# Performance work log

Measured on AMD Instinct MI355X. Metric: run time of the kernel, lower is better.

The kernel has to match this reference:

```python
import jax, jax.numpy as jnp
import numpy as np

B, N, DIM, HEADS, DH, EDGE, DEPTH, K = 4, 128, 256, 8, 64, 64, 2, 512
INNER = HEADS * DH
SCALE = DH ** -0.5


def _ln(x, g, b, eps=1e-5):
    m = x.mean(-1, keepdims=True)
    v = ((x - m) ** 2).mean(-1, keepdims=True)
    return (x - m) / jnp.sqrt(v + eps) * g + b


def _rotate_half(x):
    # interleaved pairs: (d r) with r=2 -> (-x2, x1)
    xp = x.reshape(x.shape[:-1] + (-1, 2))
    x1, x2 = xp[..., 0], xp[..., 1]
    return jnp.stack((-x2, x1), axis=-1).reshape(x.shape)


def _gated_res(x, res, gw):
    gate = jax.nn.sigmoid(jnp.concatenate((x, res, x - res), axis=-1) @ gw)
    return x * gate + res * (1 - gate)


def forward(nodes, edges, edge_ln_g, edge_ln_b, ln1_g, ln1_b, w_exp, b_exp,
            w_q, b_q, w_kv, b_kv, w_ekv, b_ekv, w_out, b_out, gate1_w,
            ln2_g, ln2_b, w_ff1, b_ff1, w_ff2, b_ff2, gate2_w, codebook):
    b, n = nodes.shape[:2]
    # LayerNorm edges over channel dim: (B,C,N,N) -> (B,N,N,C)
    e = _ln(jnp.transpose(edges, (0, 2, 3, 1)), edge_ln_g, edge_ln_b)
    # rotary frequencies over positions, repeated pairwise -> (1, N, DH)
    inv = 1.0 / (10000.0 ** (jnp.arange(0, DH, 2, dtype=jnp.float32) / DH))
    fr = jnp.repeat(jnp.arange(n, dtype=jnp.float32)[:, None] * inv[None, :], 2, axis=-1)
    cos, sin = jnp.cos(fr)[None], jnp.sin(fr)[None]

    def heads3(t):  # (B,N,H*D) -> (B*H,N,D)
        return t.reshape(b, n, HEADS, DH).transpose(0, 2, 1, 3).reshape(b * HEADS, n, DH)

    for i in range(DEPTH):
        # PreNorm + edge-conditioned attention
        x = _ln(nodes, ln1_g[i], ln1_b[i])
        x = x @ w_exp[i] + b_exp[i]
        q = x @ w_q[i] + b_q[i]
        k, v = jnp.split(x @ w_kv[i] + b_kv[i], 2, axis=-1)
        ekv = e @ w_ekv[i] + b_ekv[i]  # (B,N,N,INNER)
        q, k, v = heads3(q), heads3(k), heads3(v)
        ekv = ekv.reshape(b, n, n, HEADS, DH).transpose(0, 3, 1, 2, 4).reshape(b * HEADS, n, n, DH)
        q = q * cos + _rotate_half(q) * sin
        k = k * cos + _rotate_half(k) * sin
        kk = k[:, None, :, :] + ekv  # (BH, i, j, d)
        vv = v[:, None, :, :] + ekv
        sim = jnp.einsum('bid,bijd->bij', q, kk) * SCALE
        att = jax.nn.softmax(sim, axis=-1)
        out = jnp.einsum('bij,bijd->bid', att, vv)
        out = out.reshape(b, HEADS, n, DH).transpose(0, 2, 1, 3).reshape(b, n, INNER)
        out = out @ w_out[i] + b_out[i]
        nodes = _gated_res(out, nodes, gate1_w[i])
        # PreNorm + FeedForward
        h = _ln(nodes, ln2_g[i], ln2_b[i])
        h = jax.nn.gelu(h @ w_ff1[i] + b_ff1[i], approximate=False) @ w_ff2[i] + b_ff2[i]
        nodes = _gated_res(h, nodes, gate2_w[i])

    # VQ codebook nearest-neighbor lookup with straight-through estimator
    z = nodes.reshape(-1, DIM)
    d = (z * z).sum(-1, keepdims=True) - 2.0 * z @ codebook.T + (codebook * codebook).sum(-1)[None, :]
    idx = jnp.argmin(d, axis=-1)
    zq = codebook[idx].reshape(b, n, DIM)
    return nodes + jax.lax.stop_gradient(zq - nodes)


def setup_inputs() -> dict:
    key = jax.random.key(0)
    ks = jax.random.split(key, 16)
    s = 0.02
    inp = {
        'nodes': jax.random.normal(ks[0], (B, N, DIM), jnp.float32),
        'edges': jax.random.normal(ks[1], (B, EDGE, N, N), jnp.float32),
        'edge_ln_g': jnp.ones((EDGE,), jnp.float32),
        'edge_ln_b': jnp.zeros((EDGE,), jnp.float32),
        'ln1_g': jnp.ones((DEPTH, DIM), jnp.float32),
        'ln1_b': jnp.zeros((DEPTH, DIM), jnp.float32),
        'w_exp': s * jax.random.normal(ks[2], (DEPTH, DIM, INNER), jnp.float32),
        'b_exp': jnp.zeros((DEPTH, INNER), jnp.float32),
        'w_q': s * jax.random.normal(ks[3], (DEPTH, INNER, INNER), jnp.float32),
        'b_q': jnp.zeros((DEPTH, INNER), jnp.float32),
        'w_kv': s * jax.random.normal(ks[4], (DEPTH, INNER, 2 * INNER), jnp.float32),
        'b_kv': jnp.zeros((DEPTH, 2 * INNER), jnp.float32),
        'w_ekv': s * jax.random.normal(ks[5], (DEPTH, EDGE, INNER), jnp.float32),
        'b_ekv': jnp.zeros((DEPTH, INNER), jnp.float32),
        'w_out': s * jax.random.normal(ks[6], (DEPTH, INNER, DIM), jnp.float32),
        'b_out': jnp.zeros((DEPTH, DIM), jnp.float32),
        'gate1_w': s * jax.random.normal(ks[7], (DEPTH, 3 * DIM, 1), jnp.float32),
        'ln2_g': jnp.ones((DEPTH, DIM), jnp.float32),
        'ln2_b': jnp.zeros((DEPTH, DIM), jnp.float32),
        'w_ff1': s * jax.random.normal(ks[8], (DEPTH, DIM, 4 * DIM), jnp.float32),
        'b_ff1': jnp.zeros((DEPTH, 4 * DIM), jnp.float32),
        'w_ff2': s * jax.random.normal(ks[9], (DEPTH, 4 * DIM, DIM), jnp.float32),
        'b_ff2': jnp.zeros((DEPTH, DIM), jnp.float32),
        'gate2_w': s * jax.random.normal(ks[10], (DEPTH, 3 * DIM, 1), jnp.float32),
        'codebook': jax.random.uniform(ks[11], (K, DIM), jnp.float32, -1.0 / K, 1.0 / K),
    }
    return inp


def reference(nodes, edges, edge_ln_g, edge_ln_b, ln1_g, ln1_b, w_exp, b_exp,
              w_q, b_q, w_kv, b_kv, w_ekv, b_ekv, w_out, b_out, gate1_w,
              ln2_g, ln2_b, w_ff1, b_ff1, w_ff2, b_ff2, gate2_w, codebook):
    return forward(nodes, edges, edge_ln_g, edge_ln_b, ln1_g, ln1_b, w_exp, b_exp,
                   w_q, b_q, w_kv, b_kv, w_ekv, b_ekv, w_out, b_out, gate1_w,
                   ln2_g, ln2_b, w_ff1, b_ff1, w_ff2, b_ff2, gate2_w, codebook)
```

## Files before the change

kernel.cpp:

```cpp
#include <hip/hip_runtime.h>
#include <math.h>


#define DEV __device__ __forceinline__

constexpr int Bn = 4, Nn = 128, DIMn = 256, HEADSn = 8, DHn = 64, EDGEn = 64,
              DEPTHn = 2, Kn = 512, INNERn = 512;
constexpr int QKVW = 1536;
constexpr int PART = 131072;

DEV float wave_reduce_sum(float v) {
#pragma unroll
  for (int m = 32; m >= 1; m >>= 1) v += __shfl_xor(v, m);
  return v;
}

DEV float block_reduce_sum_256(float v, float* red) {
  v = wave_reduce_sum(v);
  int tid = threadIdx.x;
  if ((tid & 63) == 0) red[tid >> 6] = v;
  __syncthreads();
  v = red[0] + red[1] + red[2] + red[3];
  __syncthreads();
  return v;
}

DEV float gelu_exact(float x) {
  return 0.5f * x * (1.f + erff(x * 0.70710678118654752f));
}

__global__ __launch_bounds__(256) void prep_kernel(
    const float* __restrict__ edges, const float* __restrict__ eg,
    const float* __restrict__ eb, float* __restrict__ e,
    float* __restrict__ eT, float* __restrict__ cost, float* __restrict__ sint,
    const float* __restrict__ nodes_in, const float* __restrict__ ln1_g,
    const float* __restrict__ ln1_b, float* __restrict__ xln,
    float* __restrict__ nodes, const float* __restrict__ wek,
    const float* __restrict__ w_out, const float* __restrict__ bek,
    const float* __restrict__ b_out, float* __restrict__ W2,
    float* __restrict__ b_out2) {
  __shared__ float smem[8512];
  int blk = blockIdx.x;
  int tid = threadIdx.x;

  if (blk < 64) {
    int l = blk >> 5, h = (blk >> 2) & 7, nt = blk & 3;
    float* As = smem;
    float* Bs = smem + 4160;
    const float* wekl = wek + (size_t)l * 64 * 512 + h * 64;
    const float* woutl =
        w_out + (size_t)l * 512 * 256 + (size_t)(h * 64) * 256 + nt * 64;
    for (int f = tid; f < 1024; f += 256) {
      int c = f >> 4, d4 = (f & 15) << 2;
      float4 w4 = *(const float4*)(wekl + (size_t)c * 512 + d4);
      As[c * 65 + d4 + 0] = w4.x;
      As[c * 65 + d4 + 1] = w4.y;
      As[c * 65 + d4 + 2] = w4.z;
      As[c * 65 + d4 + 3] = w4.w;
    }
    for (int f = tid; f < 1024; f += 256) {
      int d = f >> 4, n4 = (f & 15) << 2;
      float4 w4 = *(const float4*)(woutl + (size_t)d * 256 + n4);
      Bs[d * 68 + n4 + 0] = w4.x;
      Bs[d * 68 + n4 + 1] = w4.y;
      Bs[d * 68 + n4 + 2] = w4.z;
      Bs[d * 68 + n4 + 3] = w4.w;
    }
    __syncthreads();
    int tx = tid & 15, ty = tid >> 4;
    float acc[4][4] = {};
    for (int d = 0; d < 64; ++d) {
      float4 bv = *(const float4*)&Bs[d * 68 + tx * 4];
#pragma unroll
      for (int u = 0; u < 4; ++u) {
        float a = As[(ty * 4 + u) * 65 + d];
        acc[u][0] += a * bv.x;
        acc[u][1] += a * bv.y;
        acc[u][2] += a * bv.z;
        acc[u][3] += a * bv.w;
      }
    }
#pragma unroll
    for (int u = 0; u < 4; ++u) {
      float4 o = {acc[u][0], acc[u][1], acc[u][2], acc[u][3]};
      *(float4*)(W2 + (size_t)l * 512 * 256 +
                 (size_t)(h * 64 + ty * 4 + u) * 256 + nt * 64 + tx * 4) = o;
    }
  } else if (blk < 72) {
    int t = blk - 64;
    int l = t >> 2, nt = t & 3;
    float* part = smem;
    int nn = tid & 63, kq = tid >> 6;
    const float* wcol = w_out + (size_t)l * 512 * 256 + nt * 64 + nn;
    float acc = 0.f;
    for (int k = kq * 128; k < kq * 128 + 128; ++k)
      acc += bek[l * 512 + k] * wcol[(size_t)k * 256];
    part[tid] = acc;
    __syncthreads();
    if (tid < 64)
      b_out2[l * 256 + nt * 64 + nn] =
          b_out[l * 256 + nt * 64 + nn] + part[nn] + part[64 + nn] +
          part[128 + nn] + part[192 + nn];
  } else if (blk < 584) {
    float* ets = smem;
    int eidx = blk - 72;
    int i = eidx & 127, b = eidx >> 7;
    int j = tid & 127;
    bool act = tid < 128;
    if (act) {
      const float* src = edges + (size_t)b * EDGEn * Nn * Nn + i * Nn + j;
      float vals[EDGEn];
      float s = 0.f;
#pragma unroll
      for (int c = 0; c < EDGEn; ++c) {
        float x = src[(size_t)c * (Nn * Nn)];
        vals[c] = x;
        s += x;
      }
      float m = s * (1.0f / 64.0f);
      float s2 = 0.f;
#pragma unroll
      for (int c = 0; c < EDGEn; ++c) {
        float d = vals[c] - m;
        s2 += d * d;
      }
      float inv = 1.f / sqrtf(s2 * (1.0f / 64.0f) + 1e-5f);
      float* dst = e + ((size_t)(b * Nn + i) * EDGEn) * Nn + j;
#pragma unroll
      for (int c = 0; c < EDGEn; ++c) {
        float o = (vals[c] - m) * inv * eg[c] + eb[c];
        dst[(size_t)c * Nn] = o;
        ets[j * 65 + c] = o;
      }
    }
    __syncthreads();
    if (act) {
      float* dstT = eT + ((size_t)(b * Nn + i) * Nn) * EDGEn;
#pragma unroll
      for (int it = 0; it < 16; ++it) {
        int f4 = it * 128 + j;
        int jj = f4 >> 4, c4 = (f4 & 15) << 2;
        float4 o4 = {ets[jj * 65 + c4], ets[jj * 65 + c4 + 1],
                     ets[jj * 65 + c4 + 2], ets[jj * 65 + c4 + 3]};
        *(float4*)(dstT + (size_t)jj * EDGEn + c4) = o4;
      }
    }
  } else if (blk < 600) {
    int t = (blk - 584) * 256 + tid;
    if (t < Nn * 32) {
      int n = t >> 5, p = t & 31;
      float inv = powf(10000.f, -(float)(2 * p) / 64.f);
      float fr = (float)n * inv;
      cost[t] = cosf(fr);
      sint[t] = sinf(fr);
    }
  } else {
    float* red = smem;
    int row = blk - 600;
    float v = nodes_in[(size_t)row * DIMn + tid];
    nodes[(size_t)row * DIMn + tid] = v;
    float m = block_reduce_sum_256(v, red) * (1.0f / 256.0f);
    float d = v - m;
    float var = block_reduce_sum_256(d * d, red) * (1.0f / 256.0f);
    float inv = 1.f / sqrtf(var + 1e-5f);
    xln[(size_t)row * DIMn + tid] = d * inv * ln1_g[tid] + ln1_b[tid];
  }
}

__global__ __launch_bounds__(256) void gemm_kernel(
    const float* __restrict__ A, const float* __restrict__ A2, int aact,
    const float* __restrict__ W1, int N1, const float* __restrict__ b1,
    const float* __restrict__ W2n, int N2, const float* __restrict__ b2,
    const float* __restrict__ Wkb, int Ksplit, float* __restrict__ C, int M,
    int Ntot, int K, int kspan, int act, const float* __restrict__ cost,
    const float* __restrict__ sint, float* __restrict__ kT) {
  __shared__ float As[32][34];
  __shared__ __align__(16) float Bs[32][68];
  int tid = threadIdx.x;
  int bx = blockIdx.x, by = blockIdx.y, zid = blockIdx.z;
  int tx = tid & 15, ty = tid >> 4;
  int arow = tid >> 3, acol = (tid & 7) << 2;
  int brow = tid >> 4, bcol = (tid & 15) << 2;
  int col0 = bx * 64;
  const float* W = W1;
  const float* bias = b1;
  int Nw = N1, wcol = col0;
  if (W2n && col0 >= N1) {
    W = W2n;
    bias = b2;
    Nw = N2;
    wcol = col0 - N1;
  }
  int kb = zid * kspan, kend = kb + kspan;
  const float* arp = A + (size_t)(by * 32 + arow) * K;
  const float* arp2 = A2 ? A2 + (size_t)(by * 32 + arow) * K : nullptr;

  auto load_a = [&](int kpos) -> float4 {
    float4 a = *(const float4*)(arp + kpos + acol);
    if (arp2) {
      float4 a2 = *(const float4*)(arp2 + kpos + acol);
      a.x += a2.x;
      a.y += a2.y;
      a.z += a2.z;
      a.w += a2.w;
    }
    if (aact == 1) {
      a.x = gelu_exact(a.x);
      a.y = gelu_exact(a.y);
      a.z = gelu_exact(a.z);
      a.w = gelu_exact(a.w);
    }
    return a;
  };

  float4 a_nxt = load_a(kb);
  const float* w0p;
  const float* w1p;
  {
    int kr0 = kb + brow, kr1 = kb + brow + 16;
    w0p = (Ksplit && kr0 >= Ksplit)
              ? Wkb + (size_t)(kr0 - Ksplit) * Nw + wcol + bcol
              : W + (size_t)kr0 * Nw + wcol + bcol;
    w1p = (Ksplit && kr1 >= Ksplit)
              ? Wkb + (size_t)(kr1 - Ksplit) * Nw + wcol + bcol
              : W + (size_t)kr1 * Nw + wcol + bcol;
  }
  float4 b0_nxt = *(const float4*)w0p;
  float4 b1_nxt = *(const float4*)w1p;

  float acc[2][4] = {};
  for (int k0 = kb; k0 < kend; k0 += 32) {
    As[acol + 0][arow] = a_nxt.x;
    As[acol + 1][arow] = a_nxt.y;
    As[acol + 2][arow] = a_nxt.z;
    As[acol + 3][arow] = a_nxt.w;
    *(float4*)&Bs[brow][bcol] = b0_nxt;
    *(float4*)&Bs[brow + 16][bcol] = b1_nxt;
    __syncthreads();
    int kn = k0 + 32;
    if (kn < kend) {
      a_nxt = load_a(kn);
      int kr0 = kn + brow, kr1 = kn + brow + 16;
      w0p = (Ksplit && kr0 >= Ksplit)
                ? Wkb + (size_t)(kr0 - Ksplit) * Nw + wcol + bcol
                : W + (size_t)kr0 * Nw + wcol + bcol;
      w1p = (Ksplit && kr1 >= Ksplit)
                ? Wkb + (size_t)(kr1 - Ksplit) * Nw + wcol + bcol
                : W + (size_t)kr1 * Nw + wcol + bcol;
      b0_nxt = *(const float4*)w0p;
      b1_nxt = *(const float4*)w1p;
    }
#pragma unroll
    for (int kk = 0; kk < 32; ++kk) {
      float2 av = *(const float2*)&As[kk][ty * 2];
      float4 bv = *(const float4*)&Bs[kk][tx * 4];
      acc[0][0] += av.x * bv.x;
      acc[0][1] += av.x * bv.y;
      acc[0][2] += av.x * bv.z;
      acc[0][3] += av.x * bv.w;
      acc[1][0] += av.y * bv.x;
      acc[1][1] += av.y * bv.y;
      acc[1][2] += av.y * bv.z;
      acc[1][3] += av.y * bv.w;
    }
    __syncthreads();
  }
  int ccol = wcol + tx * 4;
  bool ksec = (act == 4) && (col0 >= 512) && (col0 < 1024);
  float* trans = (float*)Bs;
  float* Cz = C + (size_t)zid * M * Ntot;
#pragma unroll
  for (int u = 0; u < 2; ++u) {
    int r = by * 32 + ty * 2 + u;
    float o[4];
#pragma unroll
    for (int w = 0; w < 4; ++w)
      o[w] = acc[u][w] + (zid == 0 ? bias[ccol + w] : 0.f);
    if (act == 1) {
#pragma unroll
      for (int w = 0; w < 4; ++w) o[w] = gelu_exact(o[w]);
    } else if (act == 4 && col0 < 1024) {
      int n = r & 127;
      int p0 = (ccol & 63) >> 1;
      float c0 = cost[n * 32 + p0], s0 = sint[n * 32 + p0];
      float c1 = cost[n * 32 + p0 + 1], s1 = sint[n * 32 + p0 + 1];
      float x0 = o[0], x1 = o[1], x2 = o[2], x3 = o[3];
      o[0] = x0 * c0 - x1 * s0;
      o[1] = x1 * c0 + x0 * s0;
      o[2] = x2 * c1 - x3 * s1;
      o[3] = x3 * c1 + x2 * s1;
    }
    if (ksec) {
      int jl = ty * 2 + u;
#pragma unroll
      for (int w = 0; w < 4; ++w) trans[(tx * 4 + w) * 33 + jl] = o[w];
    } else {
      float4 o4 = {o[0], o[1], o[2], o[3]};
      *(float4*)(Cz + (size_t)r * Ntot + col0 + tx * 4) = o4;
    }
  }
  if (ksec) {
    __syncthreads();
    int h = (col0 - 512) >> 6;
    int bb = (by * 32) >> 7;
#pragma unroll
    for (int q = 0; q < 2; ++q) {
      int f4 = tid * 2 + q;
      int dl = f4 >> 3, j4 = (f4 & 7) << 2;
      int jj = (by * 32 + j4) & 127;
      float4 o4 = {trans[dl * 33 + j4], trans[dl * 33 + j4 + 1],
                   trans[dl * 33 + j4 + 2], trans[dl * 33 + j4 + 3]};
      *(float4*)(kT + ((size_t)(bb * 8 + h) * 64 + dl) * 128 + jj) = o4;
    }
  }
}

__global__ __launch_bounds__(128) void attn_kernel(
    const float* __restrict__ qkv, const float* __restrict__ e,
    const float* __restrict__ eT, const float* __restrict__ kT,
    const float* __restrict__ wek, const float* __restrict__ w_out,
    const float* __restrict__ W2, float* __restrict__ proj) {
  __shared__ __align__(16) float qs[256];
  __shared__ __align__(16) float qes[256];
  __shared__ __align__(16) float att[512];
  __shared__ float avh[512];
  __shared__ float aeh[512];
  __shared__ float wekh[64 * 65];
  int blk = blockIdx.x;
  int iq = blk & 31;
  int bh = blk >> 5;
  int h = bh & 7, b = bh >> 3;
  int i0 = iq * 4;
  int row0 = b * 128 + i0;
  int tid = threadIdx.x;

  for (int f = tid; f < 256; f += 128) {
    int ii = f >> 6, d = f & 63;
    qs[f] = qkv[(size_t)(row0 + ii) * QKVW + h * 64 + d];
  }
  for (int f = tid; f < 4096; f += 128) {
    int c = f >> 6, d = f & 63;
    wekh[c * 65 + d] = wek[(size_t)c * INNERn + h * 64 + d];
  }
  __syncthreads();

  for (int f = tid; f < 256; f += 128) {
    int ii = f >> 6, c = f & 63;
    float acc = 0.f;
#pragma unroll
    for (int d = 0; d < 64; ++d) acc += qs[ii * 64 + d] * wekh[c * 65 + d];
    qes[f] = acc;
  }
  __syncthreads();

  int i2 = tid >> 5, j4 = tid & 31;
  float s0 = 0.f, s1 = 0.f, s2 = 0.f, s3 = 0.f;
  {
    const float* ktb = kT + ((size_t)bh * 64) * 128 + j4 * 4;
#pragma unroll
    for (int d4 = 0; d4 < 64; d4 += 4) {
      float4 q4 = *(const float4*)&qs[i2 * 64 + d4];
      float4 k0 = *(const float4*)(ktb + (size_t)(d4 + 0) * 128);
      float4 k1 = *(const float4*)(ktb + (size_t)(d4 + 1) * 128);
      float4 k2 = *(const float4*)(ktb + (size_t)(d4 + 2) * 128);
      float4 k3 = *(const float4*)(ktb + (size_t)(d4 + 3) * 128);
      s0 += q4.x * k0.x + q4.y * k1.x + q4.z * k2.x + q4.w * k3.x;
      s1 += q4.x * k0.y + q4.y * k1.y + q4.z * k2.y + q4.w * k3.y;
      s2 += q4.x * k0.z + q4.y * k1.z + q4.z * k2.z + q4.w * k3.z;
      s3 += q4.x * k0.w + q4.y * k1.w + q4.z * k2.w + q4.w * k3.w;
    }
    const float* eb = e + ((size_t)(row0 + i2) * 64) * 128 + j4 * 4;
#pragma unroll
    for (int c4 = 0; c4 < 64; c4 += 4) {
      float4 qe4 = *(const float4*)&qes[i2 * 64 + c4];
      float4 e0 = *(const float4*)(eb + (size_t)(c4 + 0) * 128);
      float4 e1 = *(const float4*)(eb + (size_t)(c4 + 1) * 128);
      float4 e2 = *(const float4*)(eb + (size_t)(c4 + 2) * 128);
      float4 e3 = *(const float4*)(eb + (size_t)(c4 + 3) * 128);
      s0 += qe4.x * e0.x + qe4.y * e1.x + qe4.z * e2.x + qe4.w * e3.x;
      s1 += qe4.x * e0.y + qe4.y * e1.y + qe4.z * e2.y + qe4.w * e3.y;
      s2 += qe4.x * e0.z + qe4.y * e1.z + qe4.z * e2.z + qe4.w * e3.z;
      s3 += qe4.x * e0.w + qe4.y * e1.w + qe4.z * e2.w + qe4.w * e3.w;
    }
    s0 *= 0.125f;
    s1 *= 0.125f;
    s2 *= 0.125f;
    s3 *= 0.125f;
  }
  {
    float mx = fmaxf(fmaxf(s0, s1), fmaxf(s2, s3));
#pragma unroll
    for (int m = 16; m >= 1; m >>= 1) mx = fmaxf(mx, __shfl_xor(mx, m));
    float p0 = expf(s0 - mx), p1 = expf(s1 - mx), p2 = expf(s2 - mx),
          p3 = expf(s3 - mx);
    float sm = p0 + p1 + p2 + p3;
#pragma unroll
    for (int m = 16; m >= 1; m >>= 1) sm += __shfl_xor(sm, m);
    float inv = 1.f / sm;
    float4 a4 = {p0 * inv, p1 * inv, p2 * inv, p3 * inv};
    *(float4*)&att[i2 * 128 + j4 * 4] = a4;
  }
  __syncthreads();

  {
    int d = tid & 63, half = tid >> 6;
    float av0 = 0.f, av1 = 0.f, av2 = 0.f, av3 = 0.f;
    float ae0 = 0.f, ae1 = 0.f, ae2 = 0.f, ae3 = 0.f;
    const float* vb = qkv + (size_t)(b * 128) * QKVW + 1024 + h * 64 + d;
    const float* etb = eT + ((size_t)row0 * 128) * 64 + d;
    for (int jq = 0; jq < 16; ++jq) {
      int jb = half * 64 + jq * 4;
      float4 a0 = *(const float4*)&att[0 * 128 + jb];
      float4 a1 = *(const float4*)&att[1 * 128 + jb];
      float4 a2 = *(const float4*)&att[2 * 128 + jb];
      float4 a3 = *(const float4*)&att[3 * 128 + jb];
#pragma unroll
      for (int t = 0; t < 4; ++t) {
        int j = jb + t;
        float vv = vb[(size_t)j * QKVW];
        float at0 = ((const float*)&a0)[t];
        float at1 = ((const float*)&a1)[t];
        float at2 = ((const float*)&a2)[t];
        float at3 = ((const float*)&a3)[t];
        av0 += at0 * vv;
        av1 += at1 * vv;
        av2 += at2 * vv;
        av3 += at3 * vv;
        float e0 = etb[(size_t)j * 64];
        float e1 = etb[8192 + (size_t)j * 64];
        float e2 = etb[16384 + (size_t)j * 64];
        float e3 = etb[24576 + (size_t)j * 64];
        ae0 += at0 * e0;
        ae1 += at1 * e1;
        ae2 += at2 * e2;
        ae3 += at3 * e3;
      }
    }
    avh[half * 256 + 0 * 64 + d] = av0;
    avh[half * 256 + 1 * 64 + d] = av1;
    avh[half * 256 + 2 * 64 + d] = av2;
    avh[half * 256 + 3 * 64 + d] = av3;
    aeh[half * 256 + 0 * 64 + d] = ae0;
    aeh[half * 256 + 1 * 64 + d] = ae1;
    aeh[half * 256 + 2 * 64 + d] = ae2;
    aeh[half * 256 + 3 * 64 + d] = ae3;
  }
  __syncthreads();

  for (int f = tid; f < 256; f += 128) {
    int ii = f >> 6, dd = f & 63;
    att[ii * 128 + dd] = avh[ii * 64 + dd] + avh[256 + ii * 64 + dd];
    att[ii * 128 + 64 + dd] = aeh[ii * 64 + dd] + aeh[256 + ii * 64 + dd];
  }
  __syncthreads();

  {
    int rp = tid >> 6, n4 = (tid & 63) << 2;
    int r0 = rp * 2, r1 = rp * 2 + 1;
    float o0[4] = {}, o1[4] = {};
    const float* wo = w_out + (size_t)(h * 64) * 256 + n4;
#pragma unroll 8
    for (int k = 0; k < 64; ++k) {
      float4 w4 = *(const float4*)(wo + (size_t)k * 256);
      float a0 = att[r0 * 128 + k];
      float a1 = att[r1 * 128 + k];
      o0[0] += a0 * w4.x;
      o0[1] += a0 * w4.y;
      o0[2] += a0 * w4.z;
      o0[3] += a0 * w4.w;
      o1[0] += a1 * w4.x;
      o1[1] += a1 * w4.y;
      o1[2] += a1 * w4.z;
      o1[3] += a1 * w4.w;
    }
    const float* w2 = W2 + (size_t)(h * 64) * 256 + n4;
#pragma unroll 8
    for (int k = 0; k < 64; ++k) {
      float4 w4 = *(const float4*)(w2 + (size_t)k * 256);
      float a0 = att[r0 * 128 + 64 + k];
      float a1 = att[r1 * 128 + 64 + k];
      o0[0] += a0 * w4.x;
      o0[1] += a0 * w4.y;
      o0[2] += a0 * w4.z;
      o0[3] += a0 * w4.w;
      o1[0] += a1 * w4.x;
      o1[1] += a1 * w4.y;
      o1[2] += a1 * w4.z;
      o1[3] += a1 * w4.w;
    }
    float* pp = proj + (size_t)h * PART;
    float4 v0 = {o0[0], o0[1], o0[2], o0[3]};
    float4 v1 = {o1[0], o1[1], o1[2], o1[3]};
    *(float4*)(pp + (size_t)(row0 + r0) * 256 + n4) = v0;
    *(float4*)(pp + (size_t)(row0 + r1) * 256 + n4) = v1;
  }
}

__global__ __launch_bounds__(256) void gate_ln_kernel(
    const float* __restrict__ x, int nparts, const float* __restrict__ badd,
    float* __restrict__ nodes, const float* __restrict__ gw,
    const float* __restrict__ lng, const float* __restrict__ lnb,
    float* __restrict__ xln) {
  __shared__ float red[4];
  int row = blockIdx.x, tid = threadIdx.x;
  size_t off = (size_t)row * DIMn + tid;
  float xv = x[off];
  for (int p = 1; p < nparts; ++p) xv += x[off + (size_t)p * PART];
  if (badd) xv += badd[tid];
  float rv = nodes[off];
  float pv =
      xv * gw[tid] + rv * gw[DIMn + tid] + (xv - rv) * gw[2 * DIMn + tid];
  float ssum = block_reduce_sum_256(pv, red);
  float gsig = 1.f / (1.f + expf(-ssum));
  float nv = xv * gsig + rv * (1.f - gsig);
  nodes[off] = nv;
  if (lng) {
    float m = block_reduce_sum_256(nv, red) * (1.0f / 256.0f);
    float d = nv - m;
    float var = block_reduce_sum_256(d * d, red) * (1.0f / 256.0f);
    float inv = 1.f / sqrtf(var + 1e-5f);
    xln[off] = d * inv * lng[tid] + lnb[tid];
  }
}

__global__ __launch_bounds__(256) void vq_kernel(
    const float* __restrict__ nodes, const float* __restrict__ codebook,
    float* __restrict__ out) {
  __shared__ __align__(16) float zs[4 * 256];
  __shared__ float wval[4][4];
  __shared__ int widx[4][4];
  __shared__ int fidx[4];
  int row0 = blockIdx.x * 4;
  int tid = threadIdx.x;
  for (int f = tid; f < 1024; f += 256) zs[f] = nodes[(size_t)row0 * DIMn + f];
  __syncthreads();
  int k1 = tid, k2 = tid + 256;
  const float4* c1p = (const float4*)(codebook + (size_t)k1 * DIMn);
  const float4* c2p = (const float4*)(codebook + (size_t)k2 * DIMn);
  float dot[4][2] = {};
  float cc0 = 0.f, cc1 = 0.f;
#pragma unroll 8
  for (int d4 = 0; d4 < 64; ++d4) {
    float4 c1 = c1p[d4], c2 = c2p[d4];
    cc0 += c1.x * c1.x + c1.y * c1.y + c1.z * c1.z + c1.w * c1.w;
    cc1 += c2.x * c2.x + c2.y * c2.y + c2.z * c2.z + c2.w * c2.w;
#pragma unroll
    for (int r = 0; r < 4; ++r) {
      float4 z = *(const float4*)&zs[r * 256 + d4 * 4];
      dot[r][0] += c1.x * z.x + c1.y * z.y + c1.z * z.z + c1.w * z.w;
      dot[r][1] += c2.x * z.x + c2.y * z.y + c2.z * z.z + c2.w * z.w;
    }
  }
  int lane = tid & 63, w = tid >> 6;
#pragma unroll
  for (int r = 0; r < 4; ++r) {
    float bv = cc0 - 2.f * dot[r][0];
    int bi = k1;
    float v2 = cc1 - 2.f * dot[r][1];
    if (v2 < bv) {
      bv = v2;
      bi = k2;
    }
#pragma unroll
    for (int m = 32; m >= 1; m >>= 1) {
      float ov = __shfl_xor(bv, m);
      int oi = __shfl_xor(bi, m);
      if (ov < bv || (ov == bv && oi < bi)) {
        bv = ov;
        bi = oi;
      }
    }
    if (lane == 0) {
      wval[r][w] = bv;
      widx[r][w] = bi;
    }
  }
  __syncthreads();
  if (tid < 4) {
    float bb = wval[tid][0];
    int bi = widx[tid][0];
    for (int t = 1; t < 4; ++t)
      if (wval[tid][t] < bb || (wval[tid][t] == bb && widx[tid][t] < bi)) {
        bb = wval[tid][t];
        bi = widx[tid][t];
      }
    fidx[tid] = bi;
  }
  __syncthreads();
  for (int f = tid; f < 1024; f += 256) {
    int r = f >> 8, d = f & 255;
    float zv = zs[f];
    float zq = codebook[(size_t)fidx[r] * DIMn + d];
    out[(size_t)(row0 + r) * DIMn + d] = zv + (zq - zv);
  }
}

extern "C" void kernel_launch(void* const* d_in, const int* in_sizes, int n_in,
                              void* d_out, int out_size, void* d_ws,
                              size_t ws_size, hipStream_t stream) {
  const float* nodes_in = (const float*)d_in[0];
  const float* edges = (const float*)d_in[1];
  const float* edge_ln_g = (const float*)d_in[2];
  const float* edge_ln_b = (const float*)d_in[3];
  const float* ln1_g = (const float*)d_in[4];
  const float* ln1_b = (const float*)d_in[5];
  const float* w_exp = (const float*)d_in[6];
  const float* b_exp = (const float*)d_in[7];
  const float* w_q = (const float*)d_in[8];
  const float* b_q = (const float*)d_in[9];
  const float* w_kv = (const float*)d_in[10];
  const float* b_kv = (const float*)d_in[11];
  const float* w_ekv = (const float*)d_in[12];
  const float* b_ekv = (const float*)d_in[13];
  const float* w_out = (const float*)d_in[14];
  const float* b_out = (const float*)d_in[15];
  const float* gate1_w = (const float*)d_in[16];
  const float* ln2_g = (const float*)d_in[17];
  const float* ln2_b = (const float*)d_in[18];
  const float* w_ff1 = (const float*)d_in[19];
  const float* b_ff1 = (const float*)d_in[20];
  const float* w_ff2 = (const float*)d_in[21];
  const float* b_ff2 = (const float*)d_in[22];
  const float* gate2_w = (const float*)d_in[23];
  const float* codebook = (const float*)d_in[24];

  float* ws = (float*)d_ws;
  float* e_buf = ws;
  float* eT_buf = e_buf + 4194304;
  float* cost = eT_buf + 4194304;
  float* sint = cost + 4096;
  float* nodes = sint + 4096;
  float* xln = nodes + 131072;
  float* xe = xln + 131072;
  float* qkvb = xe + 524288;
  float* kTb = qkvb + 786432;
  float* proj = kTb + 262144;
  float* ff1 = proj + 1048576;
  float* W2buf = ff1 + 1048576;
  float* bout2 = W2buf + 262144;

  prep_kernel<<<1112, 256, 0, stream>>>(
      edges, edge_ln_g, edge_ln_b, e_buf, eT_buf, cost, sint, nodes_in, ln1_g,
      ln1_b, xln, nodes, w_ekv, w_out, b_ekv, b_out, W2buf, bout2);

  for (int l = 0; l < DEPTHn; ++l) {
    gemm_kernel<<<dim3(8, 16, 2), 256, 0, stream>>>(
        xln, nullptr, 0, w_exp + l * 256 * 512, 512, b_exp + l * 512, nullptr,
        0, nullptr, nullptr, 0, xe, 512, 512, 256, 128, 0, cost, sint,
        nullptr);
    gemm_kernel<<<dim3(24, 16, 1), 256, 0, stream>>>(
        xe, xe + 262144, 0, w_q + l * 512 * 512, 512, b_q + l * 512,
        w_kv + l * 512 * 1024, 1024, b_kv + l * 1024, nullptr, 0, qkvb, 512,
        QKVW, 512, 512, 4, cost, sint, kTb);
    attn_kernel<<<1024, 128, 0, stream>>>(qkvb, e_buf, eT_buf, kTb,
                                          w_ekv + l * 64 * 512,
                                          w_out + l * 512 * 256,
                                          W2buf + l * 512 * 256, proj);
    gate_ln_kernel<<<512, 256, 0, stream>>>(
        proj, 8, bout2 + l * 256, nodes, gate1_w + l * 768, ln2_g + l * 256,
        ln2_b + l * 256, xln);
    gemm_kernel<<<dim3(16, 16, 2), 256, 0, stream>>>(
        xln, nullptr, 0, w_ff1 + l * 256 * 1024, 1024, b_ff1 + l * 1024,
        nullptr, 0, nullptr, nullptr, 0, ff1, 512, 1024, 256, 128, 0, cost,
        sint, nullptr);
    gemm_kernel<<<dim3(4, 16, 4), 256, 0, stream>>>(
        ff1, ff1 + 524288, 1, w_ff2 + l * 1024 * 256, 256, b_ff2 + l * 256,
        nullptr, 0, nullptr, nullptr, 0, proj, 512, 256, 1024, 256, 0, cost,
        sint, nullptr);
    const float* nlng = (l + 1 < DEPTHn) ? ln1_g + (l + 1) * 256 : nullptr;
    const float* nlnb = (l + 1 < DEPTHn) ? ln1_b + (l + 1) * 256 : nullptr;
    gate_ln_kernel<<<512, 256, 0, stream>>>(proj, 4, nullptr, nodes,
                                            gate2_w + l * 768, nlng, nlnb,
                                            xln);
  }
  vq_kernel<<<128, 256, 0, stream>>>(nodes, codebook, (float*)d_out);
}
```

Before: 365.9 us.

## Fold expansion projection into fused QKV weights at prep time

```diff
diff --git a/kernel.cpp b/kernel.cpp
--- a/kernel.cpp
+++ b/kernel.cpp
@@ -38,7 +38,11 @@
     float* __restrict__ nodes, const float* __restrict__ wek,
     const float* __restrict__ w_out, const float* __restrict__ bek,
     const float* __restrict__ b_out, float* __restrict__ W2,
-    float* __restrict__ b_out2) {
+    float* __restrict__ b_out2, const float* __restrict__ w_exp,
+    const float* __restrict__ b_exp, const float* __restrict__ w_q,
+    const float* __restrict__ b_q, const float* __restrict__ w_kv,
+    const float* __restrict__ b_kv, float* __restrict__ WqkvF,
+    float* __restrict__ bqkvF) {
   __shared__ float smem[8512];
   int blk = blockIdx.x;
   int tid = threadIdx.x;
@@ -154,7 +158,7 @@
       cost[t] = cosf(fr);
       sint[t] = sinf(fr);
     }
-  } else {
+  } else if (blk < 1112) {
     float* red = smem;
     int row = blk - 600;
     float v = nodes_in[(size_t)row * DIMn + tid];
@@ -164,6 +168,79 @@
     float var = block_reduce_sum_256(d * d, red) * (1.0f / 256.0f);
     float inv = 1.f / sqrtf(var + 1e-5f);
     xln[(size_t)row * DIMn + tid] = d * inv * ln1_g[tid] + ln1_b[tid];
+  } else if (blk < 1496) {
+    int t = blk - 1112;
+    int l = t / 192, r = t % 192;
+    int by = r / 24, bx = r % 24;
+    float* As = smem;
+    float* Bs = smem + 32 * 34;
+    int n0 = bx * 64;
+    const float* Aab = w_exp + (size_t)l * 256 * 512 + (size_t)(by * 32) * 512;
+    const float* Wb;
+    int ldw;
+    if (n0 < 512) {
+      Wb = w_q + (size_t)l * 512 * 512 + n0;
+      ldw = 512;
+    } else {
+      Wb = w_kv + (size_t)l * 512 * 1024 + (n0 - 512);
+      ldw = 1024;
+    }
+    int arow = tid >> 3, acol = (tid & 7) << 2;
+    int brow = tid >> 4, bcol = (tid & 15) << 2;
+    int tx = tid & 15, ty = tid >> 4;
+    float acc[2][4] = {};
+    for (int k0 = 0; k0 < 512; k0 += 32) {
+      float4 a4 = *(const float4*)(Aab + (size_t)arow * 512 + k0 + acol);
+      As[(acol + 0) * 34 + arow] = a4.x;
+      As[(acol + 1) * 34 + arow] = a4.y;
+      As[(acol + 2) * 34 + arow] = a4.z;
+      As[(acol + 3) * 34 + arow] = a4.w;
+      *(float4*)&Bs[brow * 68 + bcol] =
+          *(const float4*)(Wb + (size_t)(k0 + brow) * ldw + bcol);
+      *(float4*)&Bs[(brow + 16) * 68 + bcol] =
+          *(const float4*)(Wb + (size_t)(k0 + brow + 16) * ldw + bcol);
+      __syncthreads();
+#pragma unroll
+      for (int kk = 0; kk < 32; ++kk) {
+        float2 av = *(const float2*)&As[kk * 34 + ty * 2];
+        float4 bv = *(const float4*)&Bs[kk * 68 + tx * 4];
+        acc[0][0] += av.x * bv.x;
+        acc[0][1] += av.x * bv.y;
+        acc[0][2] += av.x * bv.z;
+        acc[0][3] += av.x * bv.w;
+        acc[1][0] += av.y * bv.x;
+        acc[1][1] += av.y * bv.y;
+        acc[1][2] += av.y * bv.z;
+        acc[1][3] += av.y * bv.w;
+      }
+      __syncthreads();
+    }
+#pragma unroll
+    for (int u = 0; u < 2; ++u) {
+      int d = by * 32 + ty * 2 + u;
+      float4 o = {acc[u][0], acc[u][1], acc[u][2], acc[u][3]};
+      *(float4*)(WqkvF + (size_t)l * 256 * 1536 + (size_t)d * 1536 + n0 +
+                 tx * 4) = o;
+    }
+  } else {
+    int t = blk - 1496;
+    int l = t / 6, seg = t % 6;
+    int n = seg * 256 + tid;
+    const float* W;
+    int ldw;
+    float acc;
+    if (n < 512) {
+      W = w_q + (size_t)l * 512 * 512 + n;
+      ldw = 512;
+      acc = b_q[l * 512 + n];
+    } else {
+      W = w_kv + (size_t)l * 512 * 1024 + (n - 512);
+      ldw = 1024;
+      acc = b_kv[l * 1024 + (n - 512)];
+    }
+    const float* be = b_exp + l * 512;
+    for (int k = 0; k < 512; ++k) acc += be[k] * W[(size_t)k * ldw];
+    bqkvF[l * 1536 + n] = acc;
   }
 }
 
@@ -291,9 +368,8 @@
       o[3] = x3 * c1 + x2 * s1;
     }
     if (ksec) {
-      int jl = ty * 2 + u;
-#pragma unroll
-      for (int w = 0; w < 4; ++w) trans[(tx * 4 + w) * 33 + jl] = o[w];
+#pragma unroll
+      for (int w = 0; w < 4; ++w) trans[(tx * 4 + w) * 33 + ty * 2 + u] = o[w];
     } else {
       float4 o4 = {o[0], o[1], o[2], o[3]};
       *(float4*)(Cz + (size_t)r * Ntot + col0 + tx * 4) = o4;
@@ -631,27 +707,25 @@
   float* sint = cost + 4096;
   float* nodes = sint + 4096;
   float* xln = nodes + 131072;
-  float* xe = xln + 131072;
-  float* qkvb = xe + 524288;
+  float* qkvb = xln + 131072;
   float* kTb = qkvb + 786432;
   float* proj = kTb + 262144;
   float* ff1 = proj + 1048576;
   float* W2buf = ff1 + 1048576;
   float* bout2 = W2buf + 262144;
-
-  prep_kernel<<<1112, 256, 0, stream>>>(
+  float* WqkvF = bout2 + 512;
+  float* bqkvF = WqkvF + 786432;
+
+  prep_kernel<<<1508, 256, 0, stream>>>(
       edges, edge_ln_g, edge_ln_b, e_buf, eT_buf, cost, sint, nodes_in, ln1_g,
-      ln1_b, xln, nodes, w_ekv, w_out, b_ekv, b_out, W2buf, bout2);
+      ln1_b, xln, nodes, w_ekv, w_out, b_ekv, b_out, W2buf, bout2, w_exp,
+      b_exp, w_q, b_q, w_kv, b_kv, WqkvF, bqkvF);
 
   for (int l = 0; l < DEPTHn; ++l) {
-    gemm_kernel<<<dim3(8, 16, 2), 256, 0, stream>>>(
-        xln, nullptr, 0, w_exp + l * 256 * 512, 512, b_exp + l * 512, nullptr,
-        0, nullptr, nullptr, 0, xe, 512, 512, 256, 128, 0, cost, sint,
-        nullptr);
     gemm_kernel<<<dim3(24, 16, 1), 256, 0, stream>>>(
-        xe, xe + 262144, 0, w_q + l * 512 * 512, 512, b_q + l * 512,
-        w_kv + l * 512 * 1024, 1024, b_kv + l * 1024, nullptr, 0, qkvb, 512,
-        QKVW, 512, 512, 4, cost, sint, kTb);
+        xln, nullptr, 0, WqkvF + (size_t)l * 256 * 1536, 1536,
+        bqkvF + l * 1536, nullptr, 0, nullptr, nullptr, 0, qkvb, 512, QKVW,
+        256, 256, 4, cost, sint, kTb);
     attn_kernel<<<1024, 128, 0, stream>>>(qkvb, e_buf, eT_buf, kTb,
                                           w_ekv + l * 64 * 512,
                                           w_out + l * 512 * 256,
```

After: 338.0 us. -7.6%, faster.
